# Optimization experiments

Measured on AMD Instinct MI355X. Metric: run time of the kernel, lower is better.

## Reference

```python
import math
import jax, jax.numpy as jnp
import numpy as np

B, T, D, S = 4, 8192, 1024, 32  # batch, seq, dim, num_slots; segment L = T // S


def setup_inputs() -> dict:
    key = jax.random.key(0)
    ks = jax.random.split(key, 11)
    d_inv_sqrt = D ** -0.5
    return {
        "x": jax.random.normal(ks[0], (B, T, D), jnp.float32),
        "gate_w": jax.random.normal(ks[1], (D, D), jnp.float32) * d_inv_sqrt,
        "gate_b": jnp.zeros((D,), jnp.float32),
        "read_q_w": jax.random.normal(ks[2], (D, D), jnp.float32) * 0.02,
        "read_k_w": jax.random.normal(ks[3], (D, D), jnp.float32) * 0.02,
        "read_v_w": jax.random.normal(ks[4], (D, D), jnp.float32) * 0.02,
        "output_w": jax.random.normal(ks[5], (D, D), jnp.float32) * d_inv_sqrt,
        "memory_slots": jax.random.normal(ks[6], (S, D), jnp.float32) * 0.02,
        "write_q_w": jax.random.normal(ks[7], (D, D), jnp.float32) * 0.02,
        "write_k_w": jax.random.normal(ks[8], (D, D), jnp.float32) * 0.02,
        "write_v_w": jax.random.normal(ks[9], (D, D), jnp.float32) * 0.02,
    }


def reference(x, gate_w, gate_b, read_q_w, read_k_w, read_v_w, output_w,
              memory_slots, write_q_w, write_k_w, write_v_w):
    b, t, d = x.shape
    s = memory_slots.shape[0]
    L = t // s  # segment length
    scale = 1.0 / math.sqrt(d)

    h = x @ gate_w.T + gate_b  # [B,T,D] gate pre-activation

    # --- write: per-slot attention over that slot's segment (block-diagonal) ---
    q = memory_slots @ write_q_w.T                      # [S,D]
    xs = x.reshape(b, s, L, d)                          # [B,S,L,D]
    k = xs @ write_k_w.T                                # [B,S,L,D]
    v = xs @ write_v_w.T                                # [B,S,L,D]
    wqk = jnp.einsum('sd,bsld->bsl', q, k) * scale      # [B,S,L]
    wattn = jax.nn.softmax(wqk, axis=-1)
    memory = jnp.einsum('bsl,bsld->bsd', wattn, v)      # [B,S,D]

    # --- read: masked cross-attention from tokens to memory slots ---
    rq = x @ read_q_w.T                                 # [B,T,D]
    rk = memory @ read_k_w.T                            # [B,S,D]
    rv = memory @ read_v_w.T                            # [B,S,D]
    rqk = jnp.einsum('btd,bsd->bts', rq, rk) * scale    # [B,T,S]
    seg = jnp.arange(t) // L                            # token -> segment index
    mask = seg[:, None] <= jnp.arange(s)[None, :]       # [T,S]; attend to slots >= own segment
    rqk = jnp.where(mask[None, :, :], rqk, -jnp.inf)
    rattn = jax.nn.softmax(rqk, axis=-1)
    read = jnp.einsum('bts,bsd->btd', rattn, rv)        # [B,T,D]

    y = x + jax.nn.sigmoid(h) * read
    out = y @ output_w.T
    return out, memory
```

## Files before the change

### kernel.cpp

```cpp
#include <hip/hip_runtime.h>
#include <stdint.h>

#define TB 4
#define TT 8192
#define TD 1024
#define TS 32
#define TL 256
#define BT 32768

typedef unsigned short u16;
typedef __bf16 bf16x8 __attribute__((ext_vector_type(8)));
typedef float f32x4 __attribute__((ext_vector_type(4)));

typedef uint32_t u32_g __attribute__((address_space(1)));
typedef uint32_t u32_l __attribute__((address_space(3)));

#define VMWAIT(N) asm volatile("s_waitcnt vmcnt(" #N ")" ::: "memory")
#define LGKM0()   asm volatile("s_waitcnt lgkmcnt(0)" ::: "memory")

__device__ __forceinline__ u16 f2b(float f){
  union { float f; uint32_t u; } a; a.f = f;
  uint32_t r = a.u + 0x7FFFu + ((a.u >> 16) & 1u);
  return (u16)(r >> 16);
}
__device__ __forceinline__ float b2f(u16 u){
  union { uint32_t u; float f; } a; a.u = ((uint32_t)u) << 16;
  return a.f;
}
__device__ __forceinline__ void gll16(const void* g, void* l){
  __builtin_amdgcn_global_load_lds((const u32_g*)g, (u32_l*)l, 16, 0, 0);
}

__global__ void k_tran(const float* __restrict__ w0, const float* __restrict__ w1,
                       const float* __restrict__ w2, const float* __restrict__ w3,
                       const float* __restrict__ ms,
                       u16* __restrict__ t0, u16* __restrict__ t1,
                       u16* __restrict__ t2, u16* __restrict__ t3,
                       u16* __restrict__ msb){
  int tid = threadIdx.x, z = blockIdx.z;
  if (z == 4){
    int i = (blockIdx.y*16 + blockIdx.x)*256 + tid;
    if (i < 8192){
      float4 v = ((const float4*)ms)[i];
      ushort4 u; u.x=f2b(v.x); u.y=f2b(v.y); u.z=f2b(v.z); u.w=f2b(v.w);
      ((ushort4*)msb)[i] = u;
    }
    return;
  }
  const float* src = (z==0)?w0:(z==1)?w1:(z==2)?w2:w3;
  u16* dst = (z==0)?t0:(z==1)?t1:(z==2)?t2:t3;
  __shared__ float sT[64][65];
  int r0 = blockIdx.y*64, c0 = blockIdx.x*64;
  int lr = tid >> 2, lc = (tid & 3)*16;
  #pragma unroll
  for (int j=0; j<4; ++j){
    float4 v = *(const float4*)(src + (size_t)(r0+lr)*TD + c0 + lc + j*4);
    sT[lr][lc+j*4+0]=v.x; sT[lr][lc+j*4+1]=v.y; sT[lr][lc+j*4+2]=v.z; sT[lr][lc+j*4+3]=v.w;
  }
  __syncthreads();
  int oc = tid >> 2, orh = (tid & 3)*16;
  #pragma unroll
  for (int j=0; j<4; ++j){
    ushort4 u;
    u.x = f2b(sT[orh+j*4+0][oc]);
    u.y = f2b(sT[orh+j*4+1][oc]);
    u.z = f2b(sT[orh+j*4+2][oc]);
    u.w = f2b(sT[orh+j*4+3][oc]);
    *(ushort4*)(dst + (size_t)(c0+oc)*TD + r0 + orh + j*4) = u;
  }
}

__global__ __launch_bounds__(512) void k_smmw(
    const u16* __restrict__ A0, const u16* __restrict__ W0, u16* __restrict__ O0, int tr0, float s0,
    const u16* __restrict__ A1, const u16* __restrict__ W1, u16* __restrict__ O1, int tr1, float s1){
  const u16 *A, *W; u16* O; int tr; float sc;
  if (blockIdx.z == 0){ A=A0; W=W0; O=O0; tr=tr0; sc=s0; }
  else                { A=A1; W=W1; O=O1; tr=tr1; sc=s1; }
  int tid = threadIdx.x, lane = tid & 63, wv = tid >> 6;
  int r15 = lane & 15, kg = lane >> 4;
  int wr = wv >> 2, wc = wv & 3;
  int m0 = blockIdx.y*128 + wr*64;
  int n0 = blockIdx.x*128 + wc*32;
  const u16* ap = A + (size_t)(m0 + r15)*TD + kg*8;
  const u16* bp = W + (size_t)(n0 + r15)*TD + kg*8;
  f32x4 acc[4][2];
  #pragma unroll
  for (int i=0;i<4;i++){ f32x4 z={0,0,0,0}; acc[i][0]=z; acc[i][1]=z; }
  #pragma unroll 2
  for (int k0=0; k0<TD; k0+=32){
    bf16x8 b0 = *(const bf16x8*)(bp + k0);
    bf16x8 b1 = *(const bf16x8*)(bp + 16*TD + k0);
    bf16x8 a0 = *(const bf16x8*)(ap + k0);
    bf16x8 a1 = *(const bf16x8*)(ap + 16*TD + k0);
    bf16x8 a2 = *(const bf16x8*)(ap + 32*TD + k0);
    bf16x8 a3 = *(const bf16x8*)(ap + 48*TD + k0);
    acc[0][0] = __builtin_amdgcn_mfma_f32_16x16x32_bf16(a0, b0, acc[0][0], 0,0,0);
    acc[0][1] = __builtin_amdgcn_mfma_f32_16x16x32_bf16(a0, b1, acc[0][1], 0,0,0);
    acc[1][0] = __builtin_amdgcn_mfma_f32_16x16x32_bf16(a1, b0, acc[1][0], 0,0,0);
    acc[1][1] = __builtin_amdgcn_mfma_f32_16x16x32_bf16(a1, b1, acc[1][1], 0,0,0);
    acc[2][0] = __builtin_amdgcn_mfma_f32_16x16x32_bf16(a2, b0, acc[2][0], 0,0,0);
    acc[2][1] = __builtin_amdgcn_mfma_f32_16x16x32_bf16(a2, b1, acc[2][1], 0,0,0);
    acc[3][0] = __builtin_amdgcn_mfma_f32_16x16x32_bf16(a3, b0, acc[3][0], 0,0,0);
    acc[3][1] = __builtin_amdgcn_mfma_f32_16x16x32_bf16(a3, b1, acc[3][1], 0,0,0);
  }
  #pragma unroll
  for (int mf=0; mf<4; ++mf){
    #pragma unroll
    for (int nf=0; nf<2; ++nf){
      int n = n0 + nf*16 + r15;
      #pragma unroll
      for (int qq=0; qq<4; ++qq){
        float v = acc[mf][nf][qq]*sc;
        int m = m0 + mf*16 + kg*4 + qq;
        if (tr) O[(size_t)n*TD + m] = f2b(v);
        else    O[(size_t)m*TD + n] = f2b(v);
      }
    }
  }
}

__global__ __launch_bounds__(512) void k_qk32(const u16* __restrict__ msb, const u16* __restrict__ WzT,
                                              float* __restrict__ qkp){
  int tid = threadIdx.x, lane = tid & 63, wv = tid >> 6;
  int r15 = lane & 15, kg = lane >> 4;
  int n0 = blockIdx.x*128 + wv*16;
  int kbase = blockIdx.y*512;
  const u16* ap = msb + (size_t)r15*TD + kbase + kg*8;
  const u16* bp = WzT + (size_t)(n0 + r15)*TD + kbase + kg*8;
  f32x4 a0 = {0,0,0,0}, a1 = {0,0,0,0};
  #pragma unroll 4
  for (int k0=0; k0<512; k0+=32){
    bf16x8 b  = *(const bf16x8*)(bp + k0);
    bf16x8 x0 = *(const bf16x8*)(ap + k0);
    bf16x8 x1 = *(const bf16x8*)(ap + 16*TD + k0);
    a0 = __builtin_amdgcn_mfma_f32_16x16x32_bf16(x0, b, a0, 0,0,0);
    a1 = __builtin_amdgcn_mfma_f32_16x16x32_bf16(x1, b, a1, 0,0,0);
  }
  const float sc = 1.0f/32.0f;
  float* o = qkp + (size_t)blockIdx.y*32768;
  #pragma unroll
  for (int qq=0; qq<4; ++qq){
    o[(size_t)(kg*4 + qq)*TD + n0 + r15]      = a0[qq]*sc;
    o[(size_t)(16 + kg*4 + qq)*TD + n0 + r15] = a1[qq]*sc;
  }
}

__global__ void k_convdot(const float* __restrict__ x, const float* __restrict__ qkp,
                          u16* __restrict__ xb, float* __restrict__ wqk,
                          const float* __restrict__ s0, const float* __restrict__ s1,
                          const float* __restrict__ s2, const float* __restrict__ s3,
                          const float* __restrict__ s4,
                          u16* __restrict__ d0, u16* __restrict__ d1,
                          u16* __restrict__ d2, u16* __restrict__ d3,
                          u16* __restrict__ d4){
  int tid = threadIdx.x;
  if (blockIdx.x >= 2048){
    int i = (blockIdx.x - 2048)*256 + tid;
    int mi = i >> 18, j = i & 262143;
    const float* src; u16* dst;
    if      (mi == 0){ src = s0; dst = d0; }
    else if (mi == 1){ src = s1; dst = d1; }
    else if (mi == 2){ src = s2; dst = d2; }
    else if (mi == 3){ src = s3; dst = d3; }
    else             { src = s4; dst = d4; }
    float4 v = ((const float4*)src)[j];
    ushort4 u; u.x=f2b(v.x); u.y=f2b(v.y); u.z=f2b(v.z); u.w=f2b(v.w);
    ((ushort4*)dst)[j] = u;
    return;
  }
  int lane = tid & 63, wv = tid >> 6;
  long bt0 = (long)blockIdx.x * 16;
  int sseg = (int)((bt0 & (TT-1)) >> 8);
  float qv[16];
  #pragma unroll
  for (int i=0;i<4;i++){
    const float* qp = qkp + (size_t)sseg*TD + i*256 + lane*4;
    float4 ta = *(const float4*)qp;
    float4 tb = *(const float4*)(qp + 32768);
    qv[i*4+0]=ta.x+tb.x; qv[i*4+1]=ta.y+tb.y; qv[i*4+2]=ta.z+tb.z; qv[i*4+3]=ta.w+tb.w;
  }
  for (int tok = wv; tok < 16; tok += 4){
    long bt = bt0 + tok;
    const float* xr = x + bt*TD;
    float dot = 0.f;
    #pragma unroll
    for (int i=0;i<4;i++){
      float4 t = *(const float4*)(xr + i*256 + lane*4);
      ushort4 u; u.x=f2b(t.x); u.y=f2b(t.y); u.z=f2b(t.z); u.w=f2b(t.w);
      *(ushort4*)(xb + bt*TD + i*256 + lane*4) = u;
      dot += t.x*qv[i*4] + t.y*qv[i*4+1] + t.z*qv[i*4+2] + t.w*qv[i*4+3];
    }
    #pragma unroll
    for (int o=32;o;o>>=1) dot += __shfl_xor(dot, o);
    if (lane == 0) wqk[bt] = dot;
  }
}

__global__ void k_wattn(const float* __restrict__ wqk, const u16* __restrict__ xb,
                        u16* __restrict__ xbarb){
  __shared__ float sw[TL];
  __shared__ float red[8];
  __shared__ f32x4 part[4][64];
  int tid = threadIdx.x, lane = tid & 63, wv = tid >> 6;
  int b = blockIdx.x >> 5, s = blockIdx.x & 31;
  long base = (long)b*TT + (long)s*TL;
  float v = wqk[base + tid];
  float m = v;
  #pragma unroll
  for (int o=32;o;o>>=1) m = fmaxf(m, __shfl_xor(m, o));
  if (lane == 0) red[wv] = m;
  __syncthreads();
  m = fmaxf(fmaxf(red[0], red[1]), fmaxf(red[2], red[3]));
  float e = __expf(v - m);
  float sm = e;
  #pragma unroll
  for (int o=32;o;o>>=1) sm += __shfl_xor(sm, o);
  if (lane == 0) red[4+wv] = sm;
  __syncthreads();
  sm = red[4]+red[5]+red[6]+red[7];
  sw[tid] = e / sm;
  __syncthreads();
  int d = blockIdx.y*256 + lane*4;
  const u16* xp = xb + (base + wv*64)*TD + d;
  f32x4 acc = {0,0,0,0};
  #pragma unroll 8
  for (int i=0; i<64; ++i){
    float w = sw[wv*64 + i];
    ushort4 u = *(const ushort4*)(xp + (size_t)i*TD);
    acc[0] += w*b2f(u.x); acc[1] += w*b2f(u.y); acc[2] += w*b2f(u.z); acc[3] += w*b2f(u.w);
  }
  part[wv][lane] = acc;
  __syncthreads();
  if (wv == 0){
    f32x4 t0 = part[0][lane], t1 = part[1][lane], t2 = part[2][lane], t3 = part[3][lane];
    ushort4 o;
    o.x = f2b(t0[0]+t1[0]+t2[0]+t3[0]);
    o.y = f2b(t0[1]+t1[1]+t2[1]+t3[1]);
    o.z = f2b(t0[2]+t1[2]+t2[2]+t3[2]);
    o.w = f2b(t0[3]+t1[3]+t2[3]+t3[3]);
    *(ushort4*)(xbarb + ((size_t)b*TS + s)*TD + d) = o;
  }
}

__global__ __launch_bounds__(512) void k_xbar3(const u16* __restrict__ xbarb,
                                               const u16* __restrict__ Wv, const u16* __restrict__ WdT,
                                               const u16* __restrict__ We,
                                               float* __restrict__ memo, u16* __restrict__ rkb,
                                               u16* __restrict__ rvT){
  int z = blockIdx.z;
  const u16* W = (z==0) ? Wv : (z==1) ? WdT : We;
  int tid = threadIdx.x, lane = tid & 63, wv = tid >> 6;
  int r15 = lane & 15, kg = lane >> 4;
  int wr = wv >> 2, wc = wv & 3;
  int n0 = blockIdx.x*128 + wc*32;
  const u16* ap = xbarb + (size_t)(wr*64 + r15)*TD + kg*8;
  const u16* bp = W + (size_t)(n0 + r15)*TD + kg*8;
  f32x4 acc[4][2];
  #pragma unroll
  for (int i=0;i<4;i++){ f32x4 zz={0,0,0,0}; acc[i][0]=zz; acc[i][1]=zz; }
  #pragma unroll 2
  for (int k0=0; k0<TD; k0+=32){
    bf16x8 b0 = *(const bf16x8*)(bp + k0);
    bf16x8 b1 = *(const bf16x8*)(bp + 16*TD + k0);
    bf16x8 a0 = *(const bf16x8*)(ap + k0);
    bf16x8 a1 = *(const bf16x8*)(ap + 16*TD + k0);
    bf16x8 a2 = *(const bf16x8*)(ap + 32*TD + k0);
    bf16x8 a3 = *(const bf16x8*)(ap + 48*TD + k0);
    acc[0][0] = __builtin_amdgcn_mfma_f32_16x16x32_bf16(a0, b0, acc[0][0], 0,0,0);
    acc[0][1] = __builtin_amdgcn_mfma_f32_16x16x32_bf16(a0, b1, acc[0][1], 0,0,0);
    acc[1][0] = __builtin_amdgcn_mfma_f32_16x16x32_bf16(a1, b0, acc[1][0], 0,0,0);
    acc[1][1] = __builtin_amdgcn_mfma_f32_16x16x32_bf16(a1, b1, acc[1][1], 0,0,0);
    acc[2][0] = __builtin_amdgcn_mfma_f32_16x16x32_bf16(a2, b0, acc[2][0], 0,0,0);
    acc[2][1] = __builtin_amdgcn_mfma_f32_16x16x32_bf16(a2, b1, acc[2][1], 0,0,0);
    acc[3][0] = __builtin_amdgcn_mfma_f32_16x16x32_bf16(a3, b0, acc[3][0], 0,0,0);
    acc[3][1] = __builtin_amdgcn_mfma_f32_16x16x32_bf16(a3, b1, acc[3][1], 0,0,0);
  }
  #pragma unroll
  for (int mf=0; mf<4; ++mf){
    #pragma unroll
    for (int nf=0; nf<2; ++nf){
      int n = n0 + nf*16 + r15;
      #pragma unroll
      for (int qq=0; qq<4; ++qq){
        float v = acc[mf][nf][qq];
        int m = wr*64 + mf*16 + kg*4 + qq;
        if (z == 0)      memo[(size_t)m*TD + n] = v;
        else if (z == 1) rkb[(size_t)m*TD + n] = f2b(v);
        else             rvT[((size_t)(m>>5)*TD + n)*TS + (m&31)] = f2b(v);
      }
    }
  }
}

__global__ __launch_bounds__(256) void k_pattn(const u16* __restrict__ xb, const u16* __restrict__ rkb,
                                               u16* __restrict__ P){
  int tid = threadIdx.x, lane = tid & 63, wv = tid >> 6;
  long bt0 = (long)blockIdx.x * 64;
  int b = (int)(bt0 >> 13);
  int smin = (int)((bt0 & (TT-1)) >> 8);
  int r15 = lane & 15, kg = lane >> 4;

  long tw = bt0 + wv*16;
  const u16* ap  = xb  + (size_t)(tw + r15)*TD + kg*8;
  const u16* bp0 = rkb + ((size_t)(b*TS + r15))*TD + kg*8;
  const u16* bp1 = rkb + ((size_t)(b*TS + 16 + r15))*TD + kg*8;
  f32x4 p0 = {0,0,0,0}, p1 = {0,0,0,0};
  #pragma unroll 4
  for (int ks=0; ks<32; ++ks){
    bf16x8 a  = *(const bf16x8*)(ap  + ks*32);
    bf16x8 b0 = *(const bf16x8*)(bp0 + ks*32);
    bf16x8 b1 = *(const bf16x8*)(bp1 + ks*32);
    p0 = __builtin_amdgcn_mfma_f32_16x16x32_bf16(a, b0, p0, 0,0,0);
    p1 = __builtin_amdgcn_mfma_f32_16x16x32_bf16(a, b1, p1, 0,0,0);
  }
  bool msk0 = (r15 < smin), msk1 = (16 + r15 < smin);
  #pragma unroll
  for (int q=0;q<4;q++){
    float l0 = msk0 ? -1e30f : p0[q];
    float l1 = msk1 ? -1e30f : p1[q];
    float mx = fmaxf(l0, l1);
    #pragma unroll
    for (int o=1;o<16;o<<=1) mx = fmaxf(mx, __shfl_xor(mx, o));
    float e0 = msk0 ? 0.f : __expf(l0 - mx);
    float e1 = msk1 ? 0.f : __expf(l1 - mx);
    float smv = e0 + e1;
    #pragma unroll
    for (int o=1;o<16;o<<=1) smv += __shfl_xor(smv, o);
    float rs = 1.f/smv;
    long trow = tw + 4*kg + q;
    P[trow*TS + r15]      = f2b(e0*rs);
    P[trow*TS + 16 + r15] = f2b(e1*rs);
  }
}

template<bool SIG>
__global__ __launch_bounds__(512, 2) void k_gemm(const u16* __restrict__ A, const u16* __restrict__ Bw,
                                                 const float* __restrict__ bias, void* __restrict__ Cp,
                                                 const u16* __restrict__ P, const u16* __restrict__ rvT){
  __shared__ __align__(16) char sL[131072];
  int tid = threadIdx.x, lane = tid & 63, wv = tid >> 6;
  int bid = blockIdx.x;
  int wg = ((bid & 7) << 6) | (bid >> 3);
  int nt = wg & 3, mt = wg >> 2;
  int m0 = mt*256, n0 = nt*256;
  int wr = wv >> 2, wc = wv & 3;
  int r15 = lane & 15, kg = lane >> 4;

  int ard[8], brd[4];
  #pragma unroll
  for (int i=0;i<8;i++){ int row = wr*128 + i*16 + r15; ard[i] = row*128 + ((kg ^ (row&7))<<4); }
  #pragma unroll
  for (int j=0;j<4;j++){ int row = wc*64  + j*16 + r15; brd[j] = row*128 + ((kg ^ (row&7))<<4); }

  const u16* asrc[4]; const u16* bsrc[4]; int ldst[4];
  #pragma unroll
  for (int r=0;r<4;r++){
    int Sp  = r*512 + tid;
    int row = Sp >> 3;
    int kq  = (Sp & 7) ^ (row & 7);
    asrc[r] = A  + (size_t)(m0 + row)*TD + kq*8;
    bsrc[r] = Bw + (size_t)(n0 + row)*TD + kq*8;
    ldst[r] = Sp*16;
  }

  f32x4 acc[8][4];
  #pragma unroll
  for (int i=0;i<8;i++){
    #pragma unroll
    for (int j=0;j<4;j++){ f32x4 z = {0,0,0,0}; acc[i][j] = z; }
  }

  auto stage = [&](int t){
    char* slot = sL + (size_t)(t&1)*65536;
    int k0 = t*64;
    #pragma unroll
    for (int r=0;r<4;r++) gll16(asrc[r] + k0, slot + ldst[r]);
    #pragma unroll
    for (int r=0;r<4;r++) gll16(bsrc[r] + k0, slot + 32768 + ldst[r]);
  };

  auto compute = [&](int t){
    const char* sa = sL + (size_t)(t&1)*65536;
    const char* sb = sa + 32768;
    bf16x8 bfg[4], af[4];
    #pragma unroll
    for (int j=0;j<4;j++) bfg[j] = *(const bf16x8*)(sb + brd[j]);
    #pragma unroll
    for (int i=0;i<4;i++) af[i] = *(const bf16x8*)(sa + ard[i]);
    LGKM0();
    __builtin_amdgcn_sched_barrier(0);
    __builtin_amdgcn_s_setprio(1);
    #pragma unroll
    for (int i=0;i<4;i++){
      #pragma unroll
      for (int j=0;j<4;j++)
        acc[i][j] = __builtin_amdgcn_mfma_f32_16x16x32_bf16(af[i], bfg[j], acc[i][j], 0,0,0);
    }
    __builtin_amdgcn_s_setprio(0);
    bf16x8 af2[4];
    #pragma unroll
    for (int i=0;i<4;i++) af2[i] = *(const bf16x8*)(sa + (ard[4+i]));
    LGKM0();
    __builtin_amdgcn_sched_barrier(0);
    __builtin_amdgcn_s_setprio(1);
    #pragma unroll
    for (int i=0;i<4;i++){
      #pragma unroll
      for (int j=0;j<4;j++)
        acc[4+i][j] = __builtin_amdgcn_mfma_f32_16x16x32_bf16(af2[i], bfg[j], acc[4+i][j], 0,0,0);
    }
    __builtin_amdgcn_s_setprio(0);
    bf16x8 bfh[4], ag[4];
    #pragma unroll
    for (int j=0;j<4;j++) bfh[j] = *(const bf16x8*)(sb + (brd[j]^64));
    #pragma unroll
    for (int i=0;i<4;i++) ag[i] = *(const bf16x8*)(sa + (ard[i]^64));
    LGKM0();
    __builtin_amdgcn_sched_barrier(0);
    __builtin_amdgcn_s_setprio(1);
    #pragma unroll
    for (int i=0;i<4;i++){
      #pragma unroll
      for (int j=0;j<4;j++)
        acc[i][j] = __builtin_amdgcn_mfma_f32_16x16x32_bf16(ag[i], bfh[j], acc[i][j], 0,0,0);
    }
    __builtin_amdgcn_s_setprio(0);
    bf16x8 ag2[4];
    #pragma unroll
    for (int i=0;i<4;i++) ag2[i] = *(const bf16x8*)(sa + (ard[4+i]^64));
    LGKM0();
    __builtin_amdgcn_sched_barrier(0);
    __builtin_amdgcn_s_setprio(1);
    #pragma unroll
    for (int i=0;i<4;i++){
      #pragma unroll
      for (int j=0;j<4;j++)
        acc[4+i][j] = __builtin_amdgcn_mfma_f32_16x16x32_bf16(ag2[i], bfh[j], acc[4+i][j], 0,0,0);
    }
    __builtin_amdgcn_s_setprio(0);
  };

  stage(0);
  for (int t=0; t<16; ++t){
    if (t > 0) __builtin_amdgcn_s_barrier();
    if (t < 15){
      stage(t+1);
      VMWAIT(8);
    } else {
      VMWAIT(0);
    }
    __builtin_amdgcn_s_barrier();
    compute(t);
  }

  if (SIG){
    int b = m0 >> 13;
    bf16x8 vfrag[4];
    #pragma unroll
    for (int j=0;j<4;j++){
      int n = n0 + wc*64 + j*16 + r15;
      vfrag[j] = *(const bf16x8*)(rvT + ((size_t)b*TD + n)*TS + kg*8);
    }
    #pragma unroll
    for (int i=0;i<8;i++){
      int tokbase = m0 + wr*128 + i*16;
      bf16x8 pfrag = *(const bf16x8*)(P + (size_t)(tokbase + r15)*TS + kg*8);
      f32x4 rd[4];
      #pragma unroll
      for (int j=0;j<4;j++){
        f32x4 z = {0,0,0,0};
        rd[j] = __builtin_amdgcn_mfma_f32_16x16x32_bf16(pfrag, vfrag[j], z, 0,0,0);
      }
      int mrow = tokbase + kg*4;
      #pragma unroll
      for (int j=0;j<4;j++){
        int n = n0 + wc*64 + j*16 + r15;
        float bj = bias[n];
        #pragma unroll
        for (int q=0;q<4;q++){
          float g = 1.f/(1.f + __expf(-(acc[i][j][q] + bj)));
          size_t idx = (size_t)(mrow + q)*TD + n;
          float xv = b2f(A[idx]);
          ((u16*)Cp)[idx] = f2b(xv + g*rd[j][q]);
        }
      }
    }
  } else {
    #pragma unroll
    for (int i=0;i<8;i++){
      int mrow = m0 + wr*128 + i*16 + kg*4;
      #pragma unroll
      for (int j=0;j<4;j++){
        int n = n0 + wc*64 + j*16 + r15;
        #pragma unroll
        for (int q=0;q<4;q++){
          size_t idx = (size_t)(mrow + q)*TD + n;
          ((float*)Cp)[idx] = acc[i][j][q];
        }
      }
    }
  }
}

extern "C" void kernel_launch(void* const* d_in, const int* in_sizes, int n_in,
                              void* d_out, int out_size, void* d_ws, size_t ws_size,
                              hipStream_t stream){
  const float* x   = (const float*)d_in[0];
  const float* gw  = (const float*)d_in[1];
  const float* gb  = (const float*)d_in[2];
  const float* rqw = (const float*)d_in[3];
  const float* rkw = (const float*)d_in[4];
  const float* rvw = (const float*)d_in[5];
  const float* ow  = (const float*)d_in[6];
  const float* ms  = (const float*)d_in[7];
  const float* wqw = (const float*)d_in[8];
  const float* wkw = (const float*)d_in[9];
  const float* wvw = (const float*)d_in[10];
  float* out = (float*)d_out;
  float* mem_out = out + (size_t)BT*TD;

  char* o = (char*)d_out;
  u16* xb    = (u16*)o;
  u16* Pb    = (u16*)(o + 67108864);
  u16* gwb   = (u16*)(o + 69206016);
  u16* wvwb  = (u16*)(o + 71303168);
  u16* rkwb  = (u16*)(o + 73400320);
  u16* rvwb  = (u16*)(o + 75497472);
  u16* xbarb = (u16*)(o + 79757312);
  u16* rvT   = (u16*)(o + 80281600);
  u16* WvT   = (u16*)(o + 84934656);
  u16* WrqT  = (u16*)(o + 87031808);
  u16* WqT   = (u16*)(o + 89128960);
  u16* WkT   = (u16*)(o + 91226112);
  u16* WhT   = (u16*)(o + 93323264);
  u16* We    = (u16*)(o + 95420416);
  u16* WdT   = (u16*)(o + 97517568);
  u16* WzT   = (u16*)(o + 99614720);
  u16* msb   = (u16*)(o + 101711872);

  char* w = (char*)d_ws;
  u16*   gy    = (u16*)(w);
  float* wqkb  = (float*)(w + 67108864);
  float* qkp   = (float*)(w + 67239936);
  u16*   rkb   = (u16*)(w + 67502080);
  u16*   owb   = (u16*)(w + 68288512);

  k_tran<<<dim3(16,16,5),256,0,stream>>>(wvw, rqw, wqw, wkw, ms, WvT, WrqT, WqT, WkT, msb);
  k_smmw<<<dim3(8,8,1),512,0,stream>>>(WqT, WkT, WzT, 1, 1.f,  WqT, WkT, WzT, 1, 1.f);
  k_qk32<<<dim3(8,2),512,0,stream>>>(msb, WzT, qkp);
  k_convdot<<<7168,256,0,stream>>>(x, qkp, xb, wqkb,
                                   gw, ow, wvw, rkw, rvw,
                                   gwb, owb, wvwb, rkwb, rvwb);
  k_wattn<<<dim3(128,4),256,0,stream>>>(wqkb, xb, xbarb);
  k_smmw<<<dim3(8,8,2),512,0,stream>>>(rkwb, WvT, WhT, 1, 1.f,  rvwb, WvT, We, 0, 1.f);
  k_smmw<<<dim3(8,8,1),512,0,stream>>>(WhT, WrqT, WdT, 1, 1.f/32.f,  WhT, WrqT, WdT, 1, 1.f/32.f);
  k_xbar3<<<dim3(8,1,3),512,0,stream>>>(xbarb, wvwb, WdT, We, mem_out, rkb, rvT);
  k_pattn<<<512,256,0,stream>>>(xb, rkb, Pb);
  k_gemm<true><<<512,512,0,stream>>>(xb, gwb, gb, gy, Pb, rvT);
  k_gemm<false><<<512,512,0,stream>>>(gy, owb, nullptr, d_out, nullptr, nullptr);
}
```

Before: 451.4 us.

## Fuse read-attention logits and softmax into gated GEMM, reassociate weight products

Removes the separate k_pattn kernel. The token-to-slot logits x·rk are now accumulated inside the gate GEMM main loop as extra MFMAs, issued by half of the waves and reusing the A fragments already in LDS. The masked softmax over the 32 slots runs in shared memory in the epilogue. The weight-product chain is also reordered (Wrk·Wrq computed earlier, merged into fewer k_smmw launches), which drops one launch. This saves a kernel launch plus the reload of xb and the P round-trip, at the cost of extra MFMA work and imbalance in the gate GEMM, more registers, and an LDS-based softmax step.

```diff
diff --git a/kernel.cpp b/kernel.cpp
--- a/kernel.cpp
+++ b/kernel.cpp
@@ -33,12 +33,12 @@
 
 __global__ void k_tran(const float* __restrict__ w0, const float* __restrict__ w1,
                        const float* __restrict__ w2, const float* __restrict__ w3,
-                       const float* __restrict__ ms,
+                       const float* __restrict__ w4, const float* __restrict__ ms,
                        u16* __restrict__ t0, u16* __restrict__ t1,
                        u16* __restrict__ t2, u16* __restrict__ t3,
-                       u16* __restrict__ msb){
+                       u16* __restrict__ t4, u16* __restrict__ msb){
   int tid = threadIdx.x, z = blockIdx.z;
-  if (z == 4){
+  if (z == 5){
     int i = (blockIdx.y*16 + blockIdx.x)*256 + tid;
     if (i < 8192){
       float4 v = ((const float4*)ms)[i];
@@ -47,8 +47,8 @@
     }
     return;
   }
-  const float* src = (z==0)?w0:(z==1)?w1:(z==2)?w2:w3;
-  u16* dst = (z==0)?t0:(z==1)?t1:(z==2)?t2:t3;
+  const float* src = (z==0)?w0:(z==1)?w1:(z==2)?w2:(z==3)?w3:w4;
+  u16* dst = (z==0)?t0:(z==1)?t1:(z==2)?t2:(z==3)?t3:t4;
   __shared__ float sT[64][65];
   int r0 = blockIdx.y*64, c0 = blockIdx.x*64;
   int lr = tid >> 2, lc = (tid & 3)*16;
@@ -292,51 +292,10 @@
   }
 }
 
-__global__ __launch_bounds__(256) void k_pattn(const u16* __restrict__ xb, const u16* __restrict__ rkb,
-                                               u16* __restrict__ P){
-  int tid = threadIdx.x, lane = tid & 63, wv = tid >> 6;
-  long bt0 = (long)blockIdx.x * 64;
-  int b = (int)(bt0 >> 13);
-  int smin = (int)((bt0 & (TT-1)) >> 8);
-  int r15 = lane & 15, kg = lane >> 4;
-
-  long tw = bt0 + wv*16;
-  const u16* ap  = xb  + (size_t)(tw + r15)*TD + kg*8;
-  const u16* bp0 = rkb + ((size_t)(b*TS + r15))*TD + kg*8;
-  const u16* bp1 = rkb + ((size_t)(b*TS + 16 + r15))*TD + kg*8;
-  f32x4 p0 = {0,0,0,0}, p1 = {0,0,0,0};
-  #pragma unroll 4
-  for (int ks=0; ks<32; ++ks){
-    bf16x8 a  = *(const bf16x8*)(ap  + ks*32);
-    bf16x8 b0 = *(const bf16x8*)(bp0 + ks*32);
-    bf16x8 b1 = *(const bf16x8*)(bp1 + ks*32);
-    p0 = __builtin_amdgcn_mfma_f32_16x16x32_bf16(a, b0, p0, 0,0,0);
-    p1 = __builtin_amdgcn_mfma_f32_16x16x32_bf16(a, b1, p1, 0,0,0);
-  }
-  bool msk0 = (r15 < smin), msk1 = (16 + r15 < smin);
-  #pragma unroll
-  for (int q=0;q<4;q++){
-    float l0 = msk0 ? -1e30f : p0[q];
-    float l1 = msk1 ? -1e30f : p1[q];
-    float mx = fmaxf(l0, l1);
-    #pragma unroll
-    for (int o=1;o<16;o<<=1) mx = fmaxf(mx, __shfl_xor(mx, o));
-    float e0 = msk0 ? 0.f : __expf(l0 - mx);
-    float e1 = msk1 ? 0.f : __expf(l1 - mx);
-    float smv = e0 + e1;
-    #pragma unroll
-    for (int o=1;o<16;o<<=1) smv += __shfl_xor(smv, o);
-    float rs = 1.f/smv;
-    long trow = tw + 4*kg + q;
-    P[trow*TS + r15]      = f2b(e0*rs);
-    P[trow*TS + 16 + r15] = f2b(e1*rs);
-  }
-}
-
 template<bool SIG>
 __global__ __launch_bounds__(512, 2) void k_gemm(const u16* __restrict__ A, const u16* __restrict__ Bw,
                                                  const float* __restrict__ bias, void* __restrict__ Cp,
-                                                 const u16* __restrict__ P, const u16* __restrict__ rvT){
+                                                 const u16* __restrict__ rkb, const u16* __restrict__ rvT){
   __shared__ __align__(16) char sL[131072];
   int tid = threadIdx.x, lane = tid & 63, wv = tid >> 6;
   int bid = blockIdx.x;
@@ -345,6 +304,8 @@
   int m0 = mt*256, n0 = nt*256;
   int wr = wv >> 2, wc = wv & 3;
   int r15 = lane & 15, kg = lane >> 4;
+  int smin = (m0 & (TT-1)) >> 8;
+  bool wcP = SIG && (wc < 2);
 
   int ard[8], brd[4];
   #pragma unroll
@@ -362,12 +323,18 @@
     bsrc[r] = Bw + (size_t)(n0 + row)*TD + kq*8;
     ldst[r] = Sp*16;
   }
+  const u16* rkp = rkb + (size_t)((m0 >> 13)*TS + (wc&1)*16 + r15)*TD + kg*8;
 
   f32x4 acc[8][4];
   #pragma unroll
   for (int i=0;i<8;i++){
     #pragma unroll
     for (int j=0;j<4;j++){ f32x4 z = {0,0,0,0}; acc[i][j] = z; }
+  }
+  f32x4 pacc[8];
+  if constexpr (SIG){
+    #pragma unroll
+    for (int i=0;i<8;i++){ f32x4 z = {0,0,0,0}; pacc[i] = z; }
   }
 
   auto stage = [&](int t){
@@ -379,7 +346,7 @@
     for (int r=0;r<4;r++) gll16(bsrc[r] + k0, slot + 32768 + ldst[r]);
   };
 
-  auto compute = [&](int t){
+  auto compute = [&](int t, bf16x8 rk0, bf16x8 rk1){
     const char* sa = sL + (size_t)(t&1)*65536;
     const char* sb = sa + 32768;
     bf16x8 bfg[4], af[4];
@@ -396,6 +363,12 @@
       for (int j=0;j<4;j++)
         acc[i][j] = __builtin_amdgcn_mfma_f32_16x16x32_bf16(af[i], bfg[j], acc[i][j], 0,0,0);
     }
+    if constexpr (SIG){
+      if (wcP){
+        #pragma unroll
+        for (int i=0;i<4;i++) pacc[i] = __builtin_amdgcn_mfma_f32_16x16x32_bf16(af[i], rk0, pacc[i], 0,0,0);
+      }
+    }
     __builtin_amdgcn_s_setprio(0);
     bf16x8 af2[4];
     #pragma unroll
@@ -409,6 +382,12 @@
       for (int j=0;j<4;j++)
         acc[4+i][j] = __builtin_amdgcn_mfma_f32_16x16x32_bf16(af2[i], bfg[j], acc[4+i][j], 0,0,0);
     }
+    if constexpr (SIG){
+      if (wcP){
+        #pragma unroll
+        for (int i=0;i<4;i++) pacc[4+i] = __builtin_amdgcn_mfma_f32_16x16x32_bf16(af2[i], rk0, pacc[4+i], 0,0,0);
+      }
+    }
     __builtin_amdgcn_s_setprio(0);
     bf16x8 bfh[4], ag[4];
     #pragma unroll
@@ -424,6 +403,12 @@
       for (int j=0;j<4;j++)
         acc[i][j] = __builtin_amdgcn_mfma_f32_16x16x32_bf16(ag[i], bfh[j], acc[i][j], 0,0,0);
     }
+    if constexpr (SIG){
+      if (wcP){
+        #pragma unroll
+        for (int i=0;i<4;i++) pacc[i] = __builtin_amdgcn_mfma_f32_16x16x32_bf16(ag[i], rk1, pacc[i], 0,0,0);
+      }
+    }
     __builtin_amdgcn_s_setprio(0);
     bf16x8 ag2[4];
     #pragma unroll
@@ -437,23 +422,70 @@
       for (int j=0;j<4;j++)
         acc[4+i][j] = __builtin_amdgcn_mfma_f32_16x16x32_bf16(ag2[i], bfh[j], acc[4+i][j], 0,0,0);
     }
+    if constexpr (SIG){
+      if (wcP){
+        #pragma unroll
+        for (int i=0;i<4;i++) pacc[4+i] = __builtin_amdgcn_mfma_f32_16x16x32_bf16(ag2[i], rk1, pacc[4+i], 0,0,0);
+      }
+    }
     __builtin_amdgcn_s_setprio(0);
   };
 
   stage(0);
   for (int t=0; t<16; ++t){
     if (t > 0) __builtin_amdgcn_s_barrier();
+    bf16x8 rk0, rk1;
+    if (wcP){
+      rk0 = *(const bf16x8*)(rkp + t*64);
+      rk1 = *(const bf16x8*)(rkp + t*64 + 32);
+      __builtin_amdgcn_sched_barrier(0);
+    }
     if (t < 15){
       stage(t+1);
       VMWAIT(8);
     } else {
       VMWAIT(0);
     }
+    __builtin_amdgcn_sched_barrier(0);
     __builtin_amdgcn_s_barrier();
-    compute(t);
-  }
-
-  if (SIG){
+    compute(t, rk0, rk1);
+  }
+
+  if constexpr (SIG){
+    float* Pf = (float*)sL;
+    u16* Pb16 = (u16*)(sL + 33792);
+    __syncthreads();
+    if (wcP){
+      #pragma unroll
+      for (int i=0;i<8;i++){
+        int tok = wr*128 + i*16 + kg*4;
+        #pragma unroll
+        for (int q=0;q<4;q++)
+          Pf[(tok+q)*33 + (wc&1)*16 + r15] = pacc[i][q];
+      }
+    }
+    __syncthreads();
+    if (tid < 256){
+      float v[32];
+      float mx = -1e30f;
+      #pragma unroll
+      for (int s=0;s<32;s++){
+        float t = Pf[tid*33 + s];
+        v[s] = t;
+        if (s >= smin) mx = fmaxf(mx, t);
+      }
+      float sum = 0.f;
+      #pragma unroll
+      for (int s=0;s<32;s++){
+        float e = (s >= smin) ? __expf(v[s]-mx) : 0.f;
+        v[s] = e; sum += e;
+      }
+      float rs = 1.f/sum;
+      #pragma unroll
+      for (int s=0;s<32;s++) Pb16[tid*40 + s] = f2b(v[s]*rs);
+    }
+    __syncthreads();
+
     int b = m0 >> 13;
     bf16x8 vfrag[4];
     #pragma unroll
@@ -463,15 +495,14 @@
     }
     #pragma unroll
     for (int i=0;i<8;i++){
-      int tokbase = m0 + wr*128 + i*16;
-      bf16x8 pfrag = *(const bf16x8*)(P + (size_t)(tokbase + r15)*TS + kg*8);
+      bf16x8 pfrag = *(const bf16x8*)(Pb16 + (wr*128 + i*16 + r15)*40 + kg*8);
       f32x4 rd[4];
       #pragma unroll
       for (int j=0;j<4;j++){
         f32x4 z = {0,0,0,0};
         rd[j] = __builtin_amdgcn_mfma_f32_16x16x32_bf16(pfrag, vfrag[j], z, 0,0,0);
       }
-      int mrow = tokbase + kg*4;
+      int mrow = m0 + wr*128 + i*16 + kg*4;
       #pragma unroll
       for (int j=0;j<4;j++){
         int n = n0 + wc*64 + j*16 + r15;
@@ -521,7 +552,6 @@
 
   char* o = (char*)d_out;
   u16* xb    = (u16*)o;
-  u16* Pb    = (u16*)(o + 67108864);
   u16* gwb   = (u16*)(o + 69206016);
   u16* wvwb  = (u16*)(o + 71303168);
   u16* rkwb  = (u16*)(o + 73400320);
@@ -532,11 +562,12 @@
   u16* WrqT  = (u16*)(o + 87031808);
   u16* WqT   = (u16*)(o + 89128960);
   u16* WkT   = (u16*)(o + 91226112);
-  u16* WhT   = (u16*)(o + 93323264);
   u16* We    = (u16*)(o + 95420416);
   u16* WdT   = (u16*)(o + 97517568);
   u16* WzT   = (u16*)(o + 99614720);
   u16* msb   = (u16*)(o + 101711872);
+  u16* WrkT  = (u16*)(o + 103809024);
+  u16* WgT   = (u16*)(o + 105906176);
 
   char* w = (char*)d_ws;
   u16*   gy    = (u16*)(w);
@@ -545,17 +576,18 @@
   u16*   rkb   = (u16*)(w + 67502080);
   u16*   owb   = (u16*)(w + 68288512);
 
-  k_tran<<<dim3(16,16,5),256,0,stream>>>(wvw, rqw, wqw, wkw, ms, WvT, WrqT, WqT, WkT, msb);
-  k_smmw<<<dim3(8,8,1),512,0,stream>>>(WqT, WkT, WzT, 1, 1.f,  WqT, WkT, WzT, 1, 1.f);
+  k_tran<<<dim3(16,16,6),256,0,stream>>>(wvw, rqw, wqw, wkw, rkw, ms,
+                                         WvT, WrqT, WqT, WkT, WrkT, msb);
+  k_smmw<<<dim3(8,8,2),512,0,stream>>>(WqT, WkT, WzT, 1, 1.f,
+                                       WrkT, WrqT, WgT, 1, 1.f/32.f);
   k_qk32<<<dim3(8,2),512,0,stream>>>(msb, WzT, qkp);
   k_convdot<<<7168,256,0,stream>>>(x, qkp, xb, wqkb,
                                    gw, ow, wvw, rkw, rvw,
                                    gwb, owb, wvwb, rkwb, rvwb);
+  k_smmw<<<dim3(8,8,2),512,0,stream>>>(rvwb, WvT, We, 0, 1.f,
+                                       WvT, WgT, WdT, 1, 1.f);
   k_wattn<<<dim3(128,4),256,0,stream>>>(wqkb, xb, xbarb);
-  k_smmw<<<dim3(8,8,2),512,0,stream>>>(rkwb, WvT, WhT, 1, 1.f,  rvwb, WvT, We, 0, 1.f);
-  k_smmw<<<dim3(8,8,1),512,0,stream>>>(WhT, WrqT, WdT, 1, 1.f/32.f,  WhT, WrqT, WdT, 1, 1.f/32.f);
   k_xbar3<<<dim3(8,1,3),512,0,stream>>>(xbarb, wvwb, WdT, We, mem_out, rkb, rvT);
-  k_pattn<<<512,256,0,stream>>>(xb, rkb, Pb);
-  k_gemm<true><<<512,512,0,stream>>>(xb, gwb, gb, gy, Pb, rvT);
+  k_gemm<true><<<512,512,0,stream>>>(xb, gwb, gb, gy, rkb, rvT);
   k_gemm<false><<<512,512,0,stream>>>(gy, owb, nullptr, d_out, nullptr, nullptr);
 }
```

Result: faster. 399.8 us (-11.4%).
